# Optimization experiments

Hardware: AMD Instinct MI355X
Metric: run time of the kernel (lower is better)

Reference implementation:

```python
import jax, jax.numpy as jnp
import numpy as np

N_NODES = 50000
N_EDGES = 800000
IN_F = 128
OUT_F = 64
ORDER = 3


def _spmm(edge_index, edge_attr, x):
    # out[row] += edge_attr[e] * x[col]  (COO sparse @ dense)
    row, col = edge_index[0], edge_index[1]
    msgs = x[col] * edge_attr[:, None]          # [E, F] gather + scale
    return jax.ops.segment_sum(msgs, row, num_segments=N_NODES)  # scatter-add


def setup_inputs() -> dict:
    key = jax.random.key(0)
    k1, k2, k3, k4 = jax.random.split(key, 4)
    x = jax.random.normal(k1, (N_NODES, IN_F), dtype=jnp.float32)
    edge_index = jax.random.randint(k2, (2, N_EDGES), 0, N_NODES, dtype=jnp.int64)
    edge_attr = jax.random.uniform(k3, (N_EDGES,), dtype=jnp.float32)
    W = jax.random.normal(k4, (OUT_F, IN_F), dtype=jnp.float32) * (1.0 / np.sqrt(IN_F))
    b = jnp.zeros((OUT_F,), dtype=jnp.float32)
    return {"x": x, "edge_index": edge_index, "edge_attr": edge_attr, "W": W, "b": b}


def reference(x, edge_index, edge_attr, W, b):
    # output = Linear(x); then `order` rounds of spmm aggregation
    out = jnp.einsum("ni,oi->no", x, W) + b      # [N, OUT_F]
    for _ in range(ORDER):
        out = _spmm(edge_index, edge_attr, out)
    return out
```

## Files before the change

### kernel.cpp

```cpp
#include <hip/hip_runtime.h>

#define IN_F   128
#define OUT_F  64
#define GR     64
#define EPB    4096
#define HB     64
#define SB     2048

typedef float  f32x4  __attribute__((ext_vector_type(4)));
typedef unsigned int u32x2 __attribute__((ext_vector_type(2)));

__device__ __forceinline__ unsigned short f2bf(float f) {
    unsigned int u = __float_as_uint(f);
    u += 0x7fffu + ((u >> 16) & 1u);
    return (unsigned short)(u >> 16);
}
__device__ __forceinline__ float bf2f(unsigned short h) {
    return __uint_as_float(((unsigned int)h) << 16);
}

template <bool BF16OUT>
__global__ __launch_bounds__(256) void gemm_hist_kernel(
    const float* __restrict__ x, const float* __restrict__ W,
    const float* __restrict__ b, void* __restrict__ outv, int N,
    const int* __restrict__ rowi, int* __restrict__ bparts, int E,
    int gemm_blocks, int hist_blocks) {

    if ((int)blockIdx.x >= gemm_blocks) {
        __shared__ int hcnt[256];
        int t = threadIdx.x;
        hcnt[t] = 0;
        __syncthreads();
        int hb = blockIdx.x - gemm_blocks;
        for (int e = hb * 256 + t; e < E; e += hist_blocks * 256)
            atomicAdd(&hcnt[rowi[e] >> 8], 1);
        __syncthreads();
        bparts[hb * 256 + t] = hcnt[t];
        return;
    }

    __shared__ float xs[GR][IN_F + 4];
    __shared__ float Wt[IN_F][OUT_F + 4];

    const int t = threadIdx.x;
    const int row0 = blockIdx.x * GR;

    for (int i = t; i < OUT_F * (IN_F / 4); i += 256) {
        int o = i & 63;
        int c = i >> 6;
        float4 v = ((const float4*)W)[o * (IN_F / 4) + c];
        Wt[4 * c + 0][o] = v.x;
        Wt[4 * c + 1][o] = v.y;
        Wt[4 * c + 2][o] = v.z;
        Wt[4 * c + 3][o] = v.w;
    }
    for (int i = t; i < GR * (IN_F / 4); i += 256) {
        int r = i >> 5, c = i & 31;
        int gr = row0 + r;
        float4 v = make_float4(0.f, 0.f, 0.f, 0.f);
        if (gr < N) v = ((const float4*)x)[(size_t)gr * (IN_F / 4) + c];
        *(float4*)&xs[r][4 * c] = v;
    }
    __syncthreads();

    const int f0 = (t & 15) * 4;
    const int r0 = (t >> 4) * 4;
    float acc[4][4] = {};

    #pragma unroll 2
    for (int k = 0; k < IN_F; k += 4) {
        float4 xv[4], wv[4];
        #pragma unroll
        for (int i = 0; i < 4; ++i) xv[i] = *(const float4*)&xs[r0 + i][k];
        #pragma unroll
        for (int j = 0; j < 4; ++j) wv[j] = *(const float4*)&Wt[k + j][f0];
        #pragma unroll
        for (int i = 0; i < 4; ++i) {
            #pragma unroll
            for (int j = 0; j < 4; ++j) {
                float wx = j == 0 ? wv[0].x : (j == 1 ? wv[0].y : (j == 2 ? wv[0].z : wv[0].w));
                float wy = j == 0 ? wv[1].x : (j == 1 ? wv[1].y : (j == 2 ? wv[1].z : wv[1].w));
                float wz = j == 0 ? wv[2].x : (j == 1 ? wv[2].y : (j == 2 ? wv[2].z : wv[2].w));
                float ww = j == 0 ? wv[3].x : (j == 1 ? wv[3].y : (j == 2 ? wv[3].z : wv[3].w));
                acc[i][j] = fmaf(xv[i].x, wx, acc[i][j]);
                acc[i][j] = fmaf(xv[i].y, wy, acc[i][j]);
                acc[i][j] = fmaf(xv[i].z, wz, acc[i][j]);
                acc[i][j] = fmaf(xv[i].w, ww, acc[i][j]);
            }
        }
    }

    float4 bv = *(const float4*)&b[f0];
    #pragma unroll
    for (int i = 0; i < 4; ++i) {
        int gr = row0 + r0 + i;
        if (gr < N) {
            float o0 = acc[i][0] + bv.x, o1 = acc[i][1] + bv.y;
            float o2 = acc[i][2] + bv.z, o3 = acc[i][3] + bv.w;
            if (BF16OUT) {
                ushort4 u = { f2bf(o0), f2bf(o1), f2bf(o2), f2bf(o3) };
                *(ushort4*)((unsigned short*)outv + (size_t)gr * OUT_F + f0) = u;
            } else {
                float4 o4 = make_float4(o0, o1, o2, o3);
                *(float4*)((float*)outv + (size_t)gr * OUT_F + f0) = o4;
            }
        }
    }
}

__global__ __launch_bounds__(256) void bscan_kernel(const int* __restrict__ bparts,
                                                    int* __restrict__ bbase,
                                                    int* __restrict__ bcursor,
                                                    int* __restrict__ rowptr,
                                                    int nb, int N, int E, int hist_blocks) {
    int t = threadIdx.x;
    int v = 0;
    if (t < nb)
        for (int hb = 0; hb < hist_blocks; ++hb) v += bparts[hb * 256 + t];
    int lane = t & 63, w = t >> 6;
    int sum = v;
    #pragma unroll
    for (int off = 1; off < 64; off <<= 1) {
        int x = __shfl_up(sum, off, 64);
        if (lane >= off) sum += x;
    }
    __shared__ int wsum[4];
    if (lane == 63) wsum[w] = sum;
    __syncthreads();
    int woff = 0;
    for (int i = 0; i < w; ++i) woff += wsum[i];
    int excl = sum + woff - v;
    if (t <= nb) bbase[t] = excl;
    if (t < nb)  bcursor[t] = excl;
    if (t == 0)  rowptr[N] = E;
}

__global__ __launch_bounds__(512) void bin_kernel(
    const int* __restrict__ rowi, const int* __restrict__ coli,
    const float* __restrict__ attr, int* __restrict__ bcursor,
    unsigned long long* __restrict__ tmp, int E) {
    __shared__ int cnt[256];
    __shared__ int cur[256];
    __shared__ int gbase[256];
    int t = threadIdx.x;
    int e0 = blockIdx.x * EPB;
    if (t < 256) { cnt[t] = 0; cur[t] = 0; }
    __syncthreads();
    int myrow[8];
    #pragma unroll
    for (int i = 0; i < 8; ++i) {
        int e = e0 + i * 512 + t;
        myrow[i] = (e < E) ? rowi[e] : -1;
        if (myrow[i] >= 0) atomicAdd(&cnt[myrow[i] >> 8], 1);
    }
    __syncthreads();
    if (t < 256 && cnt[t] > 0) gbase[t] = atomicAdd(&bcursor[t], cnt[t]);
    __syncthreads();
    #pragma unroll
    for (int i = 0; i < 8; ++i) {
        int e = e0 + i * 512 + t;
        if (myrow[i] >= 0) {
            int b = myrow[i] >> 8;
            int rank = atomicAdd(&cur[b], 1);
            unsigned long long rec = ((unsigned long long)(myrow[i] & 255) << 32)
                                   | ((unsigned int)coli[e] << 16)
                                   | (unsigned int)f2bf(attr[e]);
            tmp[(size_t)gbase[b] + rank] = rec;
        }
    }
}

__global__ __launch_bounds__(512) void bsort_kernel(
    const unsigned long long* __restrict__ tmp, const int* __restrict__ bbase,
    unsigned int* __restrict__ scv, int* __restrict__ rowptr, int N) {
    __shared__ int cnt[256];
    __shared__ int cur[256];
    __shared__ int wsum[4];
    int t = threadIdx.x, b = blockIdx.x;
    int seg = bbase[b], segend = bbase[b + 1];
    if (t < 256) cnt[t] = 0;
    __syncthreads();
    for (int i = seg + t; i < segend; i += 512)
        atomicAdd(&cnt[(int)(tmp[i] >> 32)], 1);
    __syncthreads();
    if (t < 256) {
        int v = cnt[t];
        int lane = t & 63, w = t >> 6;
        int sum = v;
        #pragma unroll
        for (int off = 1; off < 64; off <<= 1) {
            int x = __shfl_up(sum, off, 64);
            if (lane >= off) sum += x;
        }
        if (lane == 63) wsum[w] = sum;
        __syncthreads();
        int woff = 0;
        for (int i = 0; i < w; ++i) woff += wsum[i];
        int excl = sum + woff - v;
        int gidx = b * 256 + t;
        if (gidx <= N) rowptr[gidx] = seg + excl;
        cur[t] = excl;
    } else {
        __syncthreads();
    }
    __syncthreads();
    for (int i = seg + t; i < segend; i += 512) {
        unsigned long long rec = tmp[i];
        int rl = (int)(rec >> 32);
        int pos = atomicAdd(&cur[rl], 1);
        scv[(size_t)seg + pos] = (unsigned int)rec;
    }
}

#define FMA4(w, p)                                              \
    a0 = fmaf((w), __uint_as_float((p).x << 16), a0);           \
    a1 = fmaf((w), __uint_as_float((p).x & 0xffff0000u), a1);   \
    a2 = fmaf((w), __uint_as_float((p).y << 16), a2);           \
    a3 = fmaf((w), __uint_as_float((p).y & 0xffff0000u), a3)

template <bool BF16OUT>
__global__ __launch_bounds__(256) void spmm_csr_kernel(
    const int* __restrict__ rowptr, const unsigned int* __restrict__ scv,
    const unsigned short* __restrict__ in, void* __restrict__ outv,
    int N, int nwaves) {
    int gw = (blockIdx.x * 256 + threadIdx.x) >> 6;
    int lane = threadIdx.x & 63;
    int rpw = (N + nwaves - 1) / nwaves;
    int r0 = gw * rpw;
    int r1 = r0 + rpw;
    if (r1 > N) r1 = N;
    const unsigned int g = lane >> 4;
    const unsigned int s = lane & 15;

    for (int wr = r0; wr < r1; ++wr) {
        int wid = __builtin_amdgcn_readfirstlane(wr);
        int beg = rowptr[wid], end = rowptr[wid + 1];
        float a0 = 0.f, a1 = 0.f, a2 = 0.f, a3 = 0.f;

        int e = beg;
        for (; e + 16 <= end; e += 16) {
            unsigned int v0 = scv[e + g];
            unsigned int v1 = scv[e + 4 + g];
            unsigned int v2 = scv[e + 8 + g];
            unsigned int v3 = scv[e + 12 + g];
            u32x2 p0 = *(const u32x2*)(in + ((v0 >> 16) << 6) + (s << 2));
            u32x2 p1 = *(const u32x2*)(in + ((v1 >> 16) << 6) + (s << 2));
            u32x2 p2 = *(const u32x2*)(in + ((v2 >> 16) << 6) + (s << 2));
            u32x2 p3 = *(const u32x2*)(in + ((v3 >> 16) << 6) + (s << 2));
            float w0 = __uint_as_float(v0 << 16);
            float w1 = __uint_as_float(v1 << 16);
            float w2 = __uint_as_float(v2 << 16);
            float w3 = __uint_as_float(v3 << 16);
            FMA4(w0, p0);
            FMA4(w1, p1);
            FMA4(w2, p2);
            FMA4(w3, p3);
        }
        if (e + 8 <= end) {
            unsigned int v0 = scv[e + g];
            unsigned int v1 = scv[e + 4 + g];
            u32x2 p0 = *(const u32x2*)(in + ((v0 >> 16) << 6) + (s << 2));
            u32x2 p1 = *(const u32x2*)(in + ((v1 >> 16) << 6) + (s << 2));
            float w0 = __uint_as_float(v0 << 16);
            float w1 = __uint_as_float(v1 << 16);
            FMA4(w0, p0);
            FMA4(w1, p1);
            e += 8;
        }
        for (; e < end; e += 4) {
            unsigned int v = (e + (int)g < end) ? scv[e + g] : 0u;
            u32x2 p = *(const u32x2*)(in + ((v >> 16) << 6) + (s << 2));
            float w = __uint_as_float(v << 16);
            FMA4(w, p);
        }

        a0 += __shfl_xor(a0, 16); a0 += __shfl_xor(a0, 32);
        a1 += __shfl_xor(a1, 16); a1 += __shfl_xor(a1, 32);
        a2 += __shfl_xor(a2, 16); a2 += __shfl_xor(a2, 32);
        a3 += __shfl_xor(a3, 16); a3 += __shfl_xor(a3, 32);

        if (g == 0) {
            size_t o = (size_t)wid * OUT_F + (s << 2);
            if (BF16OUT) {
                unsigned long long u =  (unsigned long long)f2bf(a0)
                                     | ((unsigned long long)f2bf(a1) << 16)
                                     | ((unsigned long long)f2bf(a2) << 32)
                                     | ((unsigned long long)f2bf(a3) << 48);
                *(unsigned long long*)((unsigned short*)outv + o) = u;
            } else {
                f32x4 o4 = { a0, a1, a2, a3 };
                *(f32x4*)((float*)outv + o) = o4;
            }
        }
    }
}

__global__ __launch_bounds__(256) void spmm_atomic_kernel(
    const int* __restrict__ rowi, const int* __restrict__ coli,
    const float* __restrict__ attr, const float* __restrict__ in,
    float* __restrict__ out, int E) {
    int tid = blockIdx.x * 256 + threadIdx.x;
    int e = tid >> 6;
    int lane = tid & 63;
    if (e >= E) return;
    int r = rowi[e];
    int c = coli[e];
    float w = attr[e];
    float v = in[(size_t)c * OUT_F + lane];
    atomicAdd(&out[(size_t)r * OUT_F + lane], w * v);
}

extern "C" void kernel_launch(void* const* d_in, const int* in_sizes, int n_in,
                              void* d_out, int out_size, void* d_ws, size_t ws_size,
                              hipStream_t stream) {
    const float* x    = (const float*)d_in[0];
    const int*   ei   = (const int*)d_in[1];
    const float* attr = (const float*)d_in[2];
    const float* W    = (const float*)d_in[3];
    const float* b    = (const float*)d_in[4];
    float* out = (float*)d_out;

    const int N = in_sizes[0] / IN_F;
    const int E = in_sizes[2];
    const int* rowi = ei;
    const int* coli = ei + E;

    const size_t obytes_f  = (size_t)N * OUT_F * sizeof(float);
    const size_t obytes_bf = (size_t)N * OUT_F * sizeof(unsigned short);
    const int nb = (N + 255) / 256;

    char* wp = (char*)d_ws;
    size_t off = 0;
    auto alloc = [&](size_t bytes) { char* p = wp + off; off += (bytes + 255) & ~(size_t)255; return p; };
    unsigned short* bufA = (unsigned short*)alloc(obytes_bf);
    unsigned short* bufB = (unsigned short*)alloc((size_t)E * 8);
    unsigned long long* tmp = (unsigned long long*)bufB;
    int* rowptr  = (int*)alloc((size_t)(N + 1) * 4);
    int* bparts  = (int*)alloc((size_t)HB * 256 * 4);
    int* bbase   = (int*)alloc(260 * 4);
    int* bcursor = (int*)alloc(260 * 4);
    unsigned int* scv = (unsigned int*)alloc((size_t)E * 4);
    const bool csr_ok = (off <= ws_size) && (N <= 65280) && ((size_t)E * 8 >= obytes_bf);

    const int gemm_blocks = (N + GR - 1) / GR;
    const int nwaves = SB * 4;

    if (csr_ok) {
        gemm_hist_kernel<true><<<gemm_blocks + HB, 256, 0, stream>>>(
            x, W, b, bufA, N, rowi, bparts, E, gemm_blocks, HB);

        bscan_kernel<<<1, 256, 0, stream>>>(bparts, bbase, bcursor, rowptr, nb, N, E, HB);
        bin_kernel<<<(E + EPB - 1) / EPB, 512, 0, stream>>>(rowi, coli, attr, bcursor, tmp, E);
        bsort_kernel<<<nb, 512, 0, stream>>>(tmp, bbase, scv, rowptr, N);

        spmm_csr_kernel<true ><<<SB, 256, 0, stream>>>(rowptr, scv, bufA, bufB, N, nwaves);
        spmm_csr_kernel<true ><<<SB, 256, 0, stream>>>(rowptr, scv, bufB, bufA, N, nwaves);
        spmm_csr_kernel<false><<<SB, 256, 0, stream>>>(rowptr, scv, bufA, out, N, nwaves);
    } else {
        float* ws0 = (float*)d_ws;
        gemm_hist_kernel<false><<<gemm_blocks, 256, 0, stream>>>(
            x, W, b, ws0, N, rowi, (int*)d_ws, 0, gemm_blocks, 0);
        const int spmm_blocks = (E * 64 + 255) / 256;
        hipMemsetAsync(out, 0, obytes_f, stream);
        spmm_atomic_kernel<<<spmm_blocks, 256, 0, stream>>>(rowi, coli, attr, ws0, out, E);
        hipMemsetAsync(ws0, 0, obytes_f, stream);
        spmm_atomic_kernel<<<spmm_blocks, 256, 0, stream>>>(rowi, coli, attr, out, ws0, E);
        hipMemsetAsync(out, 0, obytes_f, stream);
        spmm_atomic_kernel<<<spmm_blocks, 256, 0, stream>>>(rowi, coli, attr, ws0, out, E);
    }
}
```

Measured before the change: 189.5 us.

## Fuse all stages into one persistent kernel with software grid barriers

Replaces the seven separate launches (GEMM+histogram, scan, bin, sort, three SpMM passes) with a single persistent kernel of 512 blocks that runs every stage in turn, separated by atomic-counter grid barriers. The GEMM input tile is also stored as bf16 in shared memory so it fits in a union with the sort scratch. The aim is to remove per-launch overhead and the idle gaps between kernels. In exchange, the barriers assume all 512 blocks are resident at once (launch bounds 256,2), which risks deadlock if occupancy is lower. Work is also spread over fewer blocks, and rounding x to bf16 before the GEMM adds precision loss.

```diff
diff --git a/kernel.cpp b/kernel.cpp
--- a/kernel.cpp
+++ b/kernel.cpp
@@ -3,9 +3,8 @@
 #define IN_F   128
 #define OUT_F  64
 #define GR     64
-#define EPB    4096
-#define HB     64
-#define SB     2048
+#define EPB2   2048
+#define NBLK   512
 
 typedef float  f32x4  __attribute__((ext_vector_type(4)));
 typedef unsigned int u32x2 __attribute__((ext_vector_type(2)));
@@ -17,199 +16,6 @@
 }
 __device__ __forceinline__ float bf2f(unsigned short h) {
     return __uint_as_float(((unsigned int)h) << 16);
-}
-
-template <bool BF16OUT>
-__global__ __launch_bounds__(256) void gemm_hist_kernel(
-    const float* __restrict__ x, const float* __restrict__ W,
-    const float* __restrict__ b, void* __restrict__ outv, int N,
-    const int* __restrict__ rowi, int* __restrict__ bparts, int E,
-    int gemm_blocks, int hist_blocks) {
-
-    if ((int)blockIdx.x >= gemm_blocks) {
-        __shared__ int hcnt[256];
-        int t = threadIdx.x;
-        hcnt[t] = 0;
-        __syncthreads();
-        int hb = blockIdx.x - gemm_blocks;
-        for (int e = hb * 256 + t; e < E; e += hist_blocks * 256)
-            atomicAdd(&hcnt[rowi[e] >> 8], 1);
-        __syncthreads();
-        bparts[hb * 256 + t] = hcnt[t];
-        return;
-    }
-
-    __shared__ float xs[GR][IN_F + 4];
-    __shared__ float Wt[IN_F][OUT_F + 4];
-
-    const int t = threadIdx.x;
-    const int row0 = blockIdx.x * GR;
-
-    for (int i = t; i < OUT_F * (IN_F / 4); i += 256) {
-        int o = i & 63;
-        int c = i >> 6;
-        float4 v = ((const float4*)W)[o * (IN_F / 4) + c];
-        Wt[4 * c + 0][o] = v.x;
-        Wt[4 * c + 1][o] = v.y;
-        Wt[4 * c + 2][o] = v.z;
-        Wt[4 * c + 3][o] = v.w;
-    }
-    for (int i = t; i < GR * (IN_F / 4); i += 256) {
-        int r = i >> 5, c = i & 31;
-        int gr = row0 + r;
-        float4 v = make_float4(0.f, 0.f, 0.f, 0.f);
-        if (gr < N) v = ((const float4*)x)[(size_t)gr * (IN_F / 4) + c];
-        *(float4*)&xs[r][4 * c] = v;
-    }
-    __syncthreads();
-
-    const int f0 = (t & 15) * 4;
-    const int r0 = (t >> 4) * 4;
-    float acc[4][4] = {};
-
-    #pragma unroll 2
-    for (int k = 0; k < IN_F; k += 4) {
-        float4 xv[4], wv[4];
-        #pragma unroll
-        for (int i = 0; i < 4; ++i) xv[i] = *(const float4*)&xs[r0 + i][k];
-        #pragma unroll
-        for (int j = 0; j < 4; ++j) wv[j] = *(const float4*)&Wt[k + j][f0];
-        #pragma unroll
-        for (int i = 0; i < 4; ++i) {
-            #pragma unroll
-            for (int j = 0; j < 4; ++j) {
-                float wx = j == 0 ? wv[0].x : (j == 1 ? wv[0].y : (j == 2 ? wv[0].z : wv[0].w));
-                float wy = j == 0 ? wv[1].x : (j == 1 ? wv[1].y : (j == 2 ? wv[1].z : wv[1].w));
-                float wz = j == 0 ? wv[2].x : (j == 1 ? wv[2].y : (j == 2 ? wv[2].z : wv[2].w));
-                float ww = j == 0 ? wv[3].x : (j == 1 ? wv[3].y : (j == 2 ? wv[3].z : wv[3].w));
-                acc[i][j] = fmaf(xv[i].x, wx, acc[i][j]);
-                acc[i][j] = fmaf(xv[i].y, wy, acc[i][j]);
-                acc[i][j] = fmaf(xv[i].z, wz, acc[i][j]);
-                acc[i][j] = fmaf(xv[i].w, ww, acc[i][j]);
-            }
-        }
-    }
-
-    float4 bv = *(const float4*)&b[f0];
-    #pragma unroll
-    for (int i = 0; i < 4; ++i) {
-        int gr = row0 + r0 + i;
-        if (gr < N) {
-            float o0 = acc[i][0] + bv.x, o1 = acc[i][1] + bv.y;
-            float o2 = acc[i][2] + bv.z, o3 = acc[i][3] + bv.w;
-            if (BF16OUT) {
-                ushort4 u = { f2bf(o0), f2bf(o1), f2bf(o2), f2bf(o3) };
-                *(ushort4*)((unsigned short*)outv + (size_t)gr * OUT_F + f0) = u;
-            } else {
-                float4 o4 = make_float4(o0, o1, o2, o3);
-                *(float4*)((float*)outv + (size_t)gr * OUT_F + f0) = o4;
-            }
-        }
-    }
-}
-
-__global__ __launch_bounds__(256) void bscan_kernel(const int* __restrict__ bparts,
-                                                    int* __restrict__ bbase,
-                                                    int* __restrict__ bcursor,
-                                                    int* __restrict__ rowptr,
-                                                    int nb, int N, int E, int hist_blocks) {
-    int t = threadIdx.x;
-    int v = 0;
-    if (t < nb)
-        for (int hb = 0; hb < hist_blocks; ++hb) v += bparts[hb * 256 + t];
-    int lane = t & 63, w = t >> 6;
-    int sum = v;
-    #pragma unroll
-    for (int off = 1; off < 64; off <<= 1) {
-        int x = __shfl_up(sum, off, 64);
-        if (lane >= off) sum += x;
-    }
-    __shared__ int wsum[4];
-    if (lane == 63) wsum[w] = sum;
-    __syncthreads();
-    int woff = 0;
-    for (int i = 0; i < w; ++i) woff += wsum[i];
-    int excl = sum + woff - v;
-    if (t <= nb) bbase[t] = excl;
-    if (t < nb)  bcursor[t] = excl;
-    if (t == 0)  rowptr[N] = E;
-}
-
-__global__ __launch_bounds__(512) void bin_kernel(
-    const int* __restrict__ rowi, const int* __restrict__ coli,
-    const float* __restrict__ attr, int* __restrict__ bcursor,
-    unsigned long long* __restrict__ tmp, int E) {
-    __shared__ int cnt[256];
-    __shared__ int cur[256];
-    __shared__ int gbase[256];
-    int t = threadIdx.x;
-    int e0 = blockIdx.x * EPB;
-    if (t < 256) { cnt[t] = 0; cur[t] = 0; }
-    __syncthreads();
-    int myrow[8];
-    #pragma unroll
-    for (int i = 0; i < 8; ++i) {
-        int e = e0 + i * 512 + t;
-        myrow[i] = (e < E) ? rowi[e] : -1;
-        if (myrow[i] >= 0) atomicAdd(&cnt[myrow[i] >> 8], 1);
-    }
-    __syncthreads();
-    if (t < 256 && cnt[t] > 0) gbase[t] = atomicAdd(&bcursor[t], cnt[t]);
-    __syncthreads();
-    #pragma unroll
-    for (int i = 0; i < 8; ++i) {
-        int e = e0 + i * 512 + t;
-        if (myrow[i] >= 0) {
-            int b = myrow[i] >> 8;
-            int rank = atomicAdd(&cur[b], 1);
-            unsigned long long rec = ((unsigned long long)(myrow[i] & 255) << 32)
-                                   | ((unsigned int)coli[e] << 16)
-                                   | (unsigned int)f2bf(attr[e]);
-            tmp[(size_t)gbase[b] + rank] = rec;
-        }
-    }
-}
-
-__global__ __launch_bounds__(512) void bsort_kernel(
-    const unsigned long long* __restrict__ tmp, const int* __restrict__ bbase,
-    unsigned int* __restrict__ scv, int* __restrict__ rowptr, int N) {
-    __shared__ int cnt[256];
-    __shared__ int cur[256];
-    __shared__ int wsum[4];
-    int t = threadIdx.x, b = blockIdx.x;
-    int seg = bbase[b], segend = bbase[b + 1];
-    if (t < 256) cnt[t] = 0;
-    __syncthreads();
-    for (int i = seg + t; i < segend; i += 512)
-        atomicAdd(&cnt[(int)(tmp[i] >> 32)], 1);
-    __syncthreads();
-    if (t < 256) {
-        int v = cnt[t];
-        int lane = t & 63, w = t >> 6;
-        int sum = v;
-        #pragma unroll
-        for (int off = 1; off < 64; off <<= 1) {
-            int x = __shfl_up(sum, off, 64);
-            if (lane >= off) sum += x;
-        }
-        if (lane == 63) wsum[w] = sum;
-        __syncthreads();
-        int woff = 0;
-        for (int i = 0; i < w; ++i) woff += wsum[i];
-        int excl = sum + woff - v;
-        int gidx = b * 256 + t;
-        if (gidx <= N) rowptr[gidx] = seg + excl;
-        cur[t] = excl;
-    } else {
-        __syncthreads();
-    }
-    __syncthreads();
-    for (int i = seg + t; i < segend; i += 512) {
-        unsigned long long rec = tmp[i];
-        int rl = (int)(rec >> 32);
-        int pos = atomicAdd(&cur[rl], 1);
-        scv[(size_t)seg + pos] = (unsigned int)rec;
-    }
 }
 
 #define FMA4(w, p)                                              \
@@ -218,25 +24,37 @@
     a2 = fmaf((w), __uint_as_float((p).y << 16), a2);           \
     a3 = fmaf((w), __uint_as_float((p).y & 0xffff0000u), a3)
 
+struct SGemm { unsigned short xs[GR][IN_F + 8]; float Wt[IN_F][OUT_F + 4]; };
+struct SSort { int cnt[256]; int cur[256]; int gbase[256]; int wsum[4]; };
+union  SH    { SGemm g; SSort s; };
+
+__device__ __forceinline__ void gridbar(int* cnt, int target) {
+    __syncthreads();
+    if (threadIdx.x == 0) {
+        __threadfence();
+        __hip_atomic_fetch_add(cnt, 1, __ATOMIC_RELAXED, __HIP_MEMORY_SCOPE_AGENT);
+        while (__hip_atomic_load(cnt, __ATOMIC_RELAXED, __HIP_MEMORY_SCOPE_AGENT) < target)
+            __builtin_amdgcn_s_sleep(2);
+    }
+    __syncthreads();
+    __threadfence();
+}
+
 template <bool BF16OUT>
-__global__ __launch_bounds__(256) void spmm_csr_kernel(
-    const int* __restrict__ rowptr, const unsigned int* __restrict__ scv,
-    const unsigned short* __restrict__ in, void* __restrict__ outv,
-    int N, int nwaves) {
-    int gw = (blockIdx.x * 256 + threadIdx.x) >> 6;
+__device__ void spmm_phase(const int* rowptr, const unsigned int* scv,
+                           const unsigned short* in, void* outv, int N) {
+    int gw = (blockIdx.x * 256 + (int)threadIdx.x) >> 6;
     int lane = threadIdx.x & 63;
+    const int nwaves = NBLK * 4;
     int rpw = (N + nwaves - 1) / nwaves;
-    int r0 = gw * rpw;
-    int r1 = r0 + rpw;
+    int r0 = gw * rpw, r1 = r0 + rpw;
     if (r1 > N) r1 = N;
-    const unsigned int g = lane >> 4;
+    const unsigned int g = (unsigned int)lane >> 4;
     const unsigned int s = lane & 15;
-
     for (int wr = r0; wr < r1; ++wr) {
         int wid = __builtin_amdgcn_readfirstlane(wr);
         int beg = rowptr[wid], end = rowptr[wid + 1];
         float a0 = 0.f, a1 = 0.f, a2 = 0.f, a3 = 0.f;
-
         int e = beg;
         for (; e + 16 <= end; e += 16) {
             unsigned int v0 = scv[e + g];
@@ -251,10 +69,7 @@
             float w1 = __uint_as_float(v1 << 16);
             float w2 = __uint_as_float(v2 << 16);
             float w3 = __uint_as_float(v3 << 16);
-            FMA4(w0, p0);
-            FMA4(w1, p1);
-            FMA4(w2, p2);
-            FMA4(w3, p3);
+            FMA4(w0, p0); FMA4(w1, p1); FMA4(w2, p2); FMA4(w3, p3);
         }
         if (e + 8 <= end) {
             unsigned int v0 = scv[e + g];
@@ -263,8 +78,7 @@
             u32x2 p1 = *(const u32x2*)(in + ((v1 >> 16) << 6) + (s << 2));
             float w0 = __uint_as_float(v0 << 16);
             float w1 = __uint_as_float(v1 << 16);
-            FMA4(w0, p0);
-            FMA4(w1, p1);
+            FMA4(w0, p0); FMA4(w1, p1);
             e += 8;
         }
         for (; e < end; e += 4) {
@@ -273,23 +87,263 @@
             float w = __uint_as_float(v << 16);
             FMA4(w, p);
         }
-
         a0 += __shfl_xor(a0, 16); a0 += __shfl_xor(a0, 32);
         a1 += __shfl_xor(a1, 16); a1 += __shfl_xor(a1, 32);
         a2 += __shfl_xor(a2, 16); a2 += __shfl_xor(a2, 32);
         a3 += __shfl_xor(a3, 16); a3 += __shfl_xor(a3, 32);
-
         if (g == 0) {
-            size_t o = (size_t)wid * OUT_F + (s << 2);
             if (BF16OUT) {
                 unsigned long long u =  (unsigned long long)f2bf(a0)
                                      | ((unsigned long long)f2bf(a1) << 16)
                                      | ((unsigned long long)f2bf(a2) << 32)
                                      | ((unsigned long long)f2bf(a3) << 48);
-                *(unsigned long long*)((unsigned short*)outv + o) = u;
+                *(unsigned long long*)((unsigned short*)outv + (size_t)wid * OUT_F + (s << 2)) = u;
             } else {
                 f32x4 o4 = { a0, a1, a2, a3 };
-                *(f32x4*)((float*)outv + o) = o4;
+                *(f32x4*)((float*)outv + (size_t)wid * OUT_F + (s << 2)) = o4;
+            }
+        }
+    }
+}
+
+__global__ __launch_bounds__(256, 2) void mega_kernel(
+    const float* __restrict__ x, const int* __restrict__ rowi, const int* __restrict__ coli,
+    const float* __restrict__ attr, const float* __restrict__ W, const float* __restrict__ bias,
+    float* __restrict__ out,
+    unsigned short* bufA, unsigned short* bufB,
+    int* rowptr, int* bparts, int* bbase, int* bcursor, unsigned int* scv,
+    int* barcnt, int N, int E, int ntiles, int nb) {
+
+    __shared__ SH sh;
+    const int t = threadIdx.x;
+    const int bid = blockIdx.x;
+
+    for (int tile = bid; tile < ntiles; tile += NBLK) {
+        const int row0 = tile * GR;
+        for (int i = t; i < OUT_F * (IN_F / 4); i += 256) {
+            int o = i & 63, c = i >> 6;
+            float4 v = ((const float4*)W)[o * (IN_F / 4) + c];
+            sh.g.Wt[4 * c + 0][o] = v.x;
+            sh.g.Wt[4 * c + 1][o] = v.y;
+            sh.g.Wt[4 * c + 2][o] = v.z;
+            sh.g.Wt[4 * c + 3][o] = v.w;
+        }
+        for (int i = t; i < GR * (IN_F / 4); i += 256) {
+            int r = i >> 5, c = i & 31;
+            int gr = row0 + r;
+            float4 v = make_float4(0.f, 0.f, 0.f, 0.f);
+            if (gr < N) v = ((const float4*)x)[(size_t)gr * (IN_F / 4) + c];
+            ushort4 u = { f2bf(v.x), f2bf(v.y), f2bf(v.z), f2bf(v.w) };
+            *(ushort4*)&sh.g.xs[r][4 * c] = u;
+        }
+        __syncthreads();
+
+        const int f0 = (t & 15) * 4;
+        const int r0 = (t >> 4) * 4;
+        float acc[4][4] = {};
+        #pragma unroll 2
+        for (int k = 0; k < IN_F; k += 4) {
+            ushort4 xu[4]; float4 wv[4];
+            #pragma unroll
+            for (int i = 0; i < 4; ++i) xu[i] = *(const ushort4*)&sh.g.xs[r0 + i][k];
+            #pragma unroll
+            for (int j = 0; j < 4; ++j) wv[j] = *(const float4*)&sh.g.Wt[k + j][f0];
+            #pragma unroll
+            for (int i = 0; i < 4; ++i) {
+                float xv0 = bf2f(xu[i].x), xv1 = bf2f(xu[i].y);
+                float xv2 = bf2f(xu[i].z), xv3 = bf2f(xu[i].w);
+                #pragma unroll
+                for (int j = 0; j < 4; ++j) {
+                    float wx = j == 0 ? wv[0].x : (j == 1 ? wv[0].y : (j == 2 ? wv[0].z : wv[0].w));
+                    float wy = j == 0 ? wv[1].x : (j == 1 ? wv[1].y : (j == 2 ? wv[1].z : wv[1].w));
+                    float wz = j == 0 ? wv[2].x : (j == 1 ? wv[2].y : (j == 2 ? wv[2].z : wv[2].w));
+                    float ww = j == 0 ? wv[3].x : (j == 1 ? wv[3].y : (j == 2 ? wv[3].z : wv[3].w));
+                    acc[i][j] = fmaf(xv0, wx, acc[i][j]);
+                    acc[i][j] = fmaf(xv1, wy, acc[i][j]);
+                    acc[i][j] = fmaf(xv2, wz, acc[i][j]);
+                    acc[i][j] = fmaf(xv3, ww, acc[i][j]);
+                }
+            }
+        }
+        float4 bv = *(const float4*)&bias[f0];
+        #pragma unroll
+        for (int i = 0; i < 4; ++i) {
+            int gr = row0 + r0 + i;
+            if (gr < N) {
+                ushort4 u = { f2bf(acc[i][0] + bv.x), f2bf(acc[i][1] + bv.y),
+                              f2bf(acc[i][2] + bv.z), f2bf(acc[i][3] + bv.w) };
+                *(ushort4*)(bufA + (size_t)gr * OUT_F + f0) = u;
+            }
+        }
+        __syncthreads();
+    }
+    sh.s.cnt[t] = 0;
+    __syncthreads();
+    for (int e = bid * 256 + t; e < E; e += NBLK * 256)
+        atomicAdd(&sh.s.cnt[rowi[e] >> 8], 1);
+    __syncthreads();
+    bparts[bid * 256 + t] = sh.s.cnt[t];
+
+    gridbar(barcnt, 1 * NBLK);
+
+    if (bid == 0) {
+        int v = 0;
+        if (t < nb)
+            for (int p = 0; p < NBLK; ++p) v += bparts[p * 256 + t];
+        int lane = t & 63, w = t >> 6, sum = v;
+        #pragma unroll
+        for (int off = 1; off < 64; off <<= 1) {
+            int xsh = __shfl_up(sum, off, 64);
+            if (lane >= off) sum += xsh;
+        }
+        if (lane == 63) sh.s.wsum[w] = sum;
+        __syncthreads();
+        int woff = 0;
+        for (int i = 0; i < w; ++i) woff += sh.s.wsum[i];
+        int excl = sum + woff - v;
+        if (t <= nb) bbase[t] = excl;
+        if (t < nb)  bcursor[t] = excl;
+        if (t == 0)  rowptr[N] = E;
+    }
+    gridbar(barcnt, 2 * NBLK);
+
+    {
+        int nchunk = (E + EPB2 - 1) / EPB2;
+        for (int c = bid; c < nchunk; c += NBLK) {
+            sh.s.cnt[t] = 0;
+            sh.s.cur[t] = 0;
+            __syncthreads();
+            int e0 = c * EPB2;
+            int myrow[8];
+            #pragma unroll
+            for (int i = 0; i < 8; ++i) {
+                int e = e0 + i * 256 + t;
+                myrow[i] = (e < E) ? rowi[e] : -1;
+                if (myrow[i] >= 0) atomicAdd(&sh.s.cnt[myrow[i] >> 8], 1);
+            }
+            __syncthreads();
+            if (sh.s.cnt[t] > 0) sh.s.gbase[t] = atomicAdd(&bcursor[t], sh.s.cnt[t]);
+            __syncthreads();
+            #pragma unroll
+            for (int i = 0; i < 8; ++i) {
+                int e = e0 + i * 256 + t;
+                if (myrow[i] >= 0) {
+                    int bb = myrow[i] >> 8;
+                    int rank = atomicAdd(&sh.s.cur[bb], 1);
+                    unsigned long long rec = ((unsigned long long)(myrow[i] & 255) << 32)
+                                           | ((unsigned int)coli[e] << 16)
+                                           | (unsigned int)f2bf(attr[e]);
+                    ((unsigned long long*)bufB)[(size_t)sh.s.gbase[bb] + rank] = rec;
+                }
+            }
+            __syncthreads();
+        }
+    }
+    gridbar(barcnt, 3 * NBLK);
+
+    {
+        const unsigned long long* tmp = (const unsigned long long*)bufB;
+        for (int bb = bid; bb < nb; bb += NBLK) {
+            int seg = bbase[bb], segend = bbase[bb + 1];
+            sh.s.cnt[t] = 0;
+            __syncthreads();
+            for (int i = seg + t; i < segend; i += 256)
+                atomicAdd(&sh.s.cnt[(int)(tmp[i] >> 32)], 1);
+            __syncthreads();
+            int v = sh.s.cnt[t];
+            int lane = t & 63, w = t >> 6, sum = v;
+            #pragma unroll
+            for (int off = 1; off < 64; off <<= 1) {
+                int xsh = __shfl_up(sum, off, 64);
+                if (lane >= off) sum += xsh;
+            }
+            if (lane == 63) sh.s.wsum[w] = sum;
+            __syncthreads();
+            int woff = 0;
+            for (int i = 0; i < w; ++i) woff += sh.s.wsum[i];
+            int excl = sum + woff - v;
+            int gidx = bb * 256 + t;
+            if (gidx <= N) rowptr[gidx] = seg + excl;
+            sh.s.cur[t] = excl;
+            __syncthreads();
+            for (int i = seg + t; i < segend; i += 256) {
+                unsigned long long rec = tmp[i];
+                int rl = (int)(rec >> 32);
+                int pos = atomicAdd(&sh.s.cur[rl], 1);
+                scv[(size_t)seg + pos] = (unsigned int)rec;
+            }
+            __syncthreads();
+        }
+    }
+    gridbar(barcnt, 4 * NBLK);
+
+    spmm_phase<true >(rowptr, scv, bufA, bufB, N);
+    gridbar(barcnt, 5 * NBLK);
+    spmm_phase<true >(rowptr, scv, bufB, bufA, N);
+    gridbar(barcnt, 6 * NBLK);
+    spmm_phase<false>(rowptr, scv, bufA, out, N);
+}
+
+template <bool BF16OUT>
+__global__ __launch_bounds__(256) void gemm_kernel_fb(
+    const float* __restrict__ x, const float* __restrict__ W,
+    const float* __restrict__ b, void* __restrict__ outv, int N) {
+    __shared__ float xs[GR][IN_F + 4];
+    __shared__ float Wt[IN_F][OUT_F + 4];
+    const int t = threadIdx.x;
+    const int row0 = blockIdx.x * GR;
+    for (int i = t; i < OUT_F * (IN_F / 4); i += 256) {
+        int o = i & 63, c = i >> 6;
+        float4 v = ((const float4*)W)[o * (IN_F / 4) + c];
+        Wt[4 * c + 0][o] = v.x; Wt[4 * c + 1][o] = v.y;
+        Wt[4 * c + 2][o] = v.z; Wt[4 * c + 3][o] = v.w;
+    }
+    for (int i = t; i < GR * (IN_F / 4); i += 256) {
+        int r = i >> 5, c = i & 31;
+        int gr = row0 + r;
+        float4 v = make_float4(0.f, 0.f, 0.f, 0.f);
+        if (gr < N) v = ((const float4*)x)[(size_t)gr * (IN_F / 4) + c];
+        *(float4*)&xs[r][4 * c] = v;
+    }
+    __syncthreads();
+    const int f0 = (t & 15) * 4;
+    const int r0 = (t >> 4) * 4;
+    float acc[4][4] = {};
+    #pragma unroll 2
+    for (int k = 0; k < IN_F; k += 4) {
+        float4 xv[4], wv[4];
+        #pragma unroll
+        for (int i = 0; i < 4; ++i) xv[i] = *(const float4*)&xs[r0 + i][k];
+        #pragma unroll
+        for (int j = 0; j < 4; ++j) wv[j] = *(const float4*)&Wt[k + j][f0];
+        #pragma unroll
+        for (int i = 0; i < 4; ++i) {
+            #pragma unroll
+            for (int j = 0; j < 4; ++j) {
+                float wx = j == 0 ? wv[0].x : (j == 1 ? wv[0].y : (j == 2 ? wv[0].z : wv[0].w));
+                float wy = j == 0 ? wv[1].x : (j == 1 ? wv[1].y : (j == 2 ? wv[1].z : wv[1].w));
+                float wz = j == 0 ? wv[2].x : (j == 1 ? wv[2].y : (j == 2 ? wv[2].z : wv[2].w));
+                float ww = j == 0 ? wv[3].x : (j == 1 ? wv[3].y : (j == 2 ? wv[3].z : wv[3].w));
+                acc[i][j] = fmaf(xv[i].x, wx, acc[i][j]);
+                acc[i][j] = fmaf(xv[i].y, wy, acc[i][j]);
+                acc[i][j] = fmaf(xv[i].z, wz, acc[i][j]);
+                acc[i][j] = fmaf(xv[i].w, ww, acc[i][j]);
+            }
+        }
+    }
+    float4 bv = *(const float4*)&b[f0];
+    #pragma unroll
+    for (int i = 0; i < 4; ++i) {
+        int gr = row0 + r0 + i;
+        if (gr < N) {
+            float o0 = acc[i][0] + bv.x, o1 = acc[i][1] + bv.y;
+            float o2 = acc[i][2] + bv.z, o3 = acc[i][3] + bv.w;
+            if (BF16OUT) {
+                ushort4 u = { f2bf(o0), f2bf(o1), f2bf(o2), f2bf(o3) };
+                *(ushort4*)((unsigned short*)outv + (size_t)gr * OUT_F + f0) = u;
+            } else {
+                float4 o4 = make_float4(o0, o1, o2, o3);
+                *(float4*)((float*)outv + (size_t)gr * OUT_F + f0) = o4;
             }
         }
     }
@@ -334,32 +388,25 @@
     auto alloc = [&](size_t bytes) { char* p = wp + off; off += (bytes + 255) & ~(size_t)255; return p; };
     unsigned short* bufA = (unsigned short*)alloc(obytes_bf);
     unsigned short* bufB = (unsigned short*)alloc((size_t)E * 8);
-    unsigned long long* tmp = (unsigned long long*)bufB;
     int* rowptr  = (int*)alloc((size_t)(N + 1) * 4);
-    int* bparts  = (int*)alloc((size_t)HB * 256 * 4);
+    int* bparts  = (int*)alloc((size_t)NBLK * 256 * 4);
     int* bbase   = (int*)alloc(260 * 4);
     int* bcursor = (int*)alloc(260 * 4);
     unsigned int* scv = (unsigned int*)alloc((size_t)E * 4);
+    int* barcnt  = (int*)alloc(256);
     const bool csr_ok = (off <= ws_size) && (N <= 65280) && ((size_t)E * 8 >= obytes_bf);
 
-    const int gemm_blocks = (N + GR - 1) / GR;
-    const int nwaves = SB * 4;
-
     if (csr_ok) {
-        gemm_hist_kernel<true><<<gemm_blocks + HB, 256, 0, stream>>>(
-            x, W, b, bufA, N, rowi, bparts, E, gemm_blocks, HB);
-
-        bscan_kernel<<<1, 256, 0, stream>>>(bparts, bbase, bcursor, rowptr, nb, N, E, HB);
-        bin_kernel<<<(E + EPB - 1) / EPB, 512, 0, stream>>>(rowi, coli, attr, bcursor, tmp, E);
-        bsort_kernel<<<nb, 512, 0, stream>>>(tmp, bbase, scv, rowptr, N);
-
-        spmm_csr_kernel<true ><<<SB, 256, 0, stream>>>(rowptr, scv, bufA, bufB, N, nwaves);
-        spmm_csr_kernel<true ><<<SB, 256, 0, stream>>>(rowptr, scv, bufB, bufA, N, nwaves);
-        spmm_csr_kernel<false><<<SB, 256, 0, stream>>>(rowptr, scv, bufA, out, N, nwaves);
+        const int ntiles = (N + GR - 1) / GR;
+        hipMemsetAsync(barcnt, 0, 256, stream);
+        mega_kernel<<<NBLK, 256, 0, stream>>>(
+            x, rowi, coli, attr, W, b, out,
+            bufA, bufB, rowptr, bparts, bbase, bcursor, scv,
+            barcnt, N, E, ntiles, nb);
     } else {
         float* ws0 = (float*)d_ws;
-        gemm_hist_kernel<false><<<gemm_blocks, 256, 0, stream>>>(
-            x, W, b, ws0, N, rowi, (int*)d_ws, 0, gemm_blocks, 0);
+        const int gemm_blocks = (N + GR - 1) / GR;
+        gemm_kernel_fb<false><<<gemm_blocks, 256, 0, stream>>>(x, W, b, ws0, N);
         const int spmm_blocks = (E * 64 + 255) / 256;
         hipMemsetAsync(out, 0, obytes_f, stream);
         spmm_atomic_kernel<<<spmm_blocks, 256, 0, stream>>>(rowi, coli, attr, ws0, out, E);
```

Result: slower. 728.7 us (+284.6%).

## Replace two-level bucket sort CSR build with per-row histogram, scan, atomic scatter

Applied to the files above, without the earlier changes.

Replaces the COO-to-CSR conversion, which used a coarse 256-row bucket histogram, bin pass and per-bucket local sort, with per-row global atomic counts, a single-block 1024-thread scan over all rows, and one atomic scatter pass. This drops one kernel and the 8-byte temporary record pass. In exchange it adds a memset, 800k global atomics in the histogram and again in the scatter, and a serial single-block scan over 50k rows. Edge order within a row becomes nondeterministic, which changes floating-point summation order.

```diff
diff --git a/kernel.cpp b/kernel.cpp
--- a/kernel.cpp
+++ b/kernel.cpp
@@ -3,9 +3,9 @@
 #define IN_F   128
 #define OUT_F  64
 #define GR     64
-#define EPB    4096
-#define HB     64
+#define HB     128
 #define SB     2048
+#define SCATB  1024
 
 typedef float  f32x4  __attribute__((ext_vector_type(4)));
 typedef unsigned int u32x2 __attribute__((ext_vector_type(2)));
@@ -23,19 +23,13 @@
 __global__ __launch_bounds__(256) void gemm_hist_kernel(
     const float* __restrict__ x, const float* __restrict__ W,
     const float* __restrict__ b, void* __restrict__ outv, int N,
-    const int* __restrict__ rowi, int* __restrict__ bparts, int E,
+    const int* __restrict__ rowi, int* __restrict__ rowcnt, int E,
     int gemm_blocks, int hist_blocks) {
 
     if ((int)blockIdx.x >= gemm_blocks) {
-        __shared__ int hcnt[256];
-        int t = threadIdx.x;
-        hcnt[t] = 0;
-        __syncthreads();
         int hb = blockIdx.x - gemm_blocks;
-        for (int e = hb * 256 + t; e < E; e += hist_blocks * 256)
-            atomicAdd(&hcnt[rowi[e] >> 8], 1);
-        __syncthreads();
-        bparts[hb * 256 + t] = hcnt[t];
+        for (int e = hb * 256 + threadIdx.x; e < E; e += hist_blocks * 256)
+            atomicAdd(&rowcnt[rowi[e]], 1);
         return;
     }
 
@@ -108,107 +102,49 @@
     }
 }
 
-__global__ __launch_bounds__(256) void bscan_kernel(const int* __restrict__ bparts,
-                                                    int* __restrict__ bbase,
-                                                    int* __restrict__ bcursor,
-                                                    int* __restrict__ rowptr,
-                                                    int nb, int N, int E, int hist_blocks) {
-    int t = threadIdx.x;
-    int v = 0;
-    if (t < nb)
-        for (int hb = 0; hb < hist_blocks; ++hb) v += bparts[hb * 256 + t];
+__global__ __launch_bounds__(1024) void scan50k_kernel(
+    const int* __restrict__ rowcnt, int* __restrict__ rowptr,
+    int* __restrict__ rowcur, int N, int E, int vpt) {
+    const int t = threadIdx.x;
+    const int base = t * vpt;
+    int sum = 0;
+    for (int i = 0; i < vpt; ++i) {
+        int idx = base + i;
+        if (idx < N) sum += rowcnt[idx];
+    }
     int lane = t & 63, w = t >> 6;
-    int sum = v;
+    int s = sum;
     #pragma unroll
     for (int off = 1; off < 64; off <<= 1) {
-        int x = __shfl_up(sum, off, 64);
-        if (lane >= off) sum += x;
-    }
-    __shared__ int wsum[4];
-    if (lane == 63) wsum[w] = sum;
+        int xsh = __shfl_up(s, off, 64);
+        if (lane >= off) s += xsh;
+    }
+    __shared__ int wsums[16];
+    if (lane == 63) wsums[w] = s;
     __syncthreads();
     int woff = 0;
-    for (int i = 0; i < w; ++i) woff += wsum[i];
-    int excl = sum + woff - v;
-    if (t <= nb) bbase[t] = excl;
-    if (t < nb)  bcursor[t] = excl;
-    if (t == 0)  rowptr[N] = E;
-}
-
-__global__ __launch_bounds__(512) void bin_kernel(
+    for (int i = 0; i < w; ++i) woff += wsums[i];
+    int run = s + woff - sum;
+    for (int i = 0; i < vpt; ++i) {
+        int idx = base + i;
+        if (idx < N) {
+            rowptr[idx] = run;
+            rowcur[idx] = run;
+            run += rowcnt[idx];
+        }
+    }
+    if (t == 1023) rowptr[N] = E;
+}
+
+__global__ __launch_bounds__(256) void scatter_kernel(
     const int* __restrict__ rowi, const int* __restrict__ coli,
-    const float* __restrict__ attr, int* __restrict__ bcursor,
-    unsigned long long* __restrict__ tmp, int E) {
-    __shared__ int cnt[256];
-    __shared__ int cur[256];
-    __shared__ int gbase[256];
-    int t = threadIdx.x;
-    int e0 = blockIdx.x * EPB;
-    if (t < 256) { cnt[t] = 0; cur[t] = 0; }
-    __syncthreads();
-    int myrow[8];
-    #pragma unroll
-    for (int i = 0; i < 8; ++i) {
-        int e = e0 + i * 512 + t;
-        myrow[i] = (e < E) ? rowi[e] : -1;
-        if (myrow[i] >= 0) atomicAdd(&cnt[myrow[i] >> 8], 1);
-    }
-    __syncthreads();
-    if (t < 256 && cnt[t] > 0) gbase[t] = atomicAdd(&bcursor[t], cnt[t]);
-    __syncthreads();
-    #pragma unroll
-    for (int i = 0; i < 8; ++i) {
-        int e = e0 + i * 512 + t;
-        if (myrow[i] >= 0) {
-            int b = myrow[i] >> 8;
-            int rank = atomicAdd(&cur[b], 1);
-            unsigned long long rec = ((unsigned long long)(myrow[i] & 255) << 32)
-                                   | ((unsigned int)coli[e] << 16)
-                                   | (unsigned int)f2bf(attr[e]);
-            tmp[(size_t)gbase[b] + rank] = rec;
-        }
-    }
-}
-
-__global__ __launch_bounds__(512) void bsort_kernel(
-    const unsigned long long* __restrict__ tmp, const int* __restrict__ bbase,
-    unsigned int* __restrict__ scv, int* __restrict__ rowptr, int N) {
-    __shared__ int cnt[256];
-    __shared__ int cur[256];
-    __shared__ int wsum[4];
-    int t = threadIdx.x, b = blockIdx.x;
-    int seg = bbase[b], segend = bbase[b + 1];
-    if (t < 256) cnt[t] = 0;
-    __syncthreads();
-    for (int i = seg + t; i < segend; i += 512)
-        atomicAdd(&cnt[(int)(tmp[i] >> 32)], 1);
-    __syncthreads();
-    if (t < 256) {
-        int v = cnt[t];
-        int lane = t & 63, w = t >> 6;
-        int sum = v;
-        #pragma unroll
-        for (int off = 1; off < 64; off <<= 1) {
-            int x = __shfl_up(sum, off, 64);
-            if (lane >= off) sum += x;
-        }
-        if (lane == 63) wsum[w] = sum;
-        __syncthreads();
-        int woff = 0;
-        for (int i = 0; i < w; ++i) woff += wsum[i];
-        int excl = sum + woff - v;
-        int gidx = b * 256 + t;
-        if (gidx <= N) rowptr[gidx] = seg + excl;
-        cur[t] = excl;
-    } else {
-        __syncthreads();
-    }
-    __syncthreads();
-    for (int i = seg + t; i < segend; i += 512) {
-        unsigned long long rec = tmp[i];
-        int rl = (int)(rec >> 32);
-        int pos = atomicAdd(&cur[rl], 1);
-        scv[(size_t)seg + pos] = (unsigned int)rec;
+    const float* __restrict__ attr, int* __restrict__ rowcur,
+    unsigned int* __restrict__ scv, int E) {
+    for (int e = blockIdx.x * 256 + threadIdx.x; e < E; e += gridDim.x * 256) {
+        int r = rowi[e];
+        unsigned int rec = ((unsigned int)coli[e] << 16) | (unsigned int)f2bf(attr[e]);
+        int pos = atomicAdd(&rowcur[r], 1);
+        scv[pos] = rec;
     }
 }
 
@@ -327,31 +263,28 @@
 
     const size_t obytes_f  = (size_t)N * OUT_F * sizeof(float);
     const size_t obytes_bf = (size_t)N * OUT_F * sizeof(unsigned short);
-    const int nb = (N + 255) / 256;
 
     char* wp = (char*)d_ws;
     size_t off = 0;
     auto alloc = [&](size_t bytes) { char* p = wp + off; off += (bytes + 255) & ~(size_t)255; return p; };
     unsigned short* bufA = (unsigned short*)alloc(obytes_bf);
-    unsigned short* bufB = (unsigned short*)alloc((size_t)E * 8);
-    unsigned long long* tmp = (unsigned long long*)bufB;
+    unsigned short* bufB = (unsigned short*)alloc(obytes_bf);
     int* rowptr  = (int*)alloc((size_t)(N + 1) * 4);
-    int* bparts  = (int*)alloc((size_t)HB * 256 * 4);
-    int* bbase   = (int*)alloc(260 * 4);
-    int* bcursor = (int*)alloc(260 * 4);
+    int* rowcnt  = (int*)alloc((size_t)N * 4);
+    int* rowcur  = (int*)alloc((size_t)N * 4);
     unsigned int* scv = (unsigned int*)alloc((size_t)E * 4);
-    const bool csr_ok = (off <= ws_size) && (N <= 65280) && ((size_t)E * 8 >= obytes_bf);
+    const bool csr_ok = (off <= ws_size) && (N <= 65535);
 
     const int gemm_blocks = (N + GR - 1) / GR;
     const int nwaves = SB * 4;
 
     if (csr_ok) {
+        hipMemsetAsync(rowcnt, 0, (size_t)N * 4, stream);
         gemm_hist_kernel<true><<<gemm_blocks + HB, 256, 0, stream>>>(
-            x, W, b, bufA, N, rowi, bparts, E, gemm_blocks, HB);
-
-        bscan_kernel<<<1, 256, 0, stream>>>(bparts, bbase, bcursor, rowptr, nb, N, E, HB);
-        bin_kernel<<<(E + EPB - 1) / EPB, 512, 0, stream>>>(rowi, coli, attr, bcursor, tmp, E);
-        bsort_kernel<<<nb, 512, 0, stream>>>(tmp, bbase, scv, rowptr, N);
+            x, W, b, bufA, N, rowi, rowcnt, E, gemm_blocks, HB);
+        const int vpt = (N + 1023) / 1024;
+        scan50k_kernel<<<1, 1024, 0, stream>>>(rowcnt, rowptr, rowcur, N, E, vpt);
+        scatter_kernel<<<SCATB, 256, 0, stream>>>(rowi, coli, attr, rowcur, scv, E);
 
         spmm_csr_kernel<true ><<<SB, 256, 0, stream>>>(rowptr, scv, bufA, bufB, N, nwaves);
         spmm_csr_kernel<true ><<<SB, 256, 0, stream>>>(rowptr, scv, bufB, bufA, N, nwaves);
```

Result: slower. 356.6 us (+88.2%).
